# Kernel optimization log

Measured on AMD Instinct MI355X. Metric: run time of the kernel, lower is better.

The kernel has to match this reference:

```python
import jax, jax.numpy as jnp
import numpy as np

B, S, E, NH = 4, 1024, 512, 8
D = E // NH

def layer_norm(x, scale, bias, eps=1e-5):
    mu = jnp.mean(x, -1, keepdims=True)
    var = jnp.mean((x - mu) ** 2, -1, keepdims=True)
    return (x - mu) * jax.lax.rsqrt(var + eps) * scale + bias

def mha(qx, kx, vx, qw, qb, kw, kb, vw, vb, ow, ob, temp):
    b, sq, e = qx.shape
    sk = kx.shape[1]
    q = (qx @ qw + qb).reshape(b, sq, NH, D)
    k = (kx @ kw + kb).reshape(b, sk, NH, D)
    v = (vx @ vw + vb).reshape(b, sk, NH, D)
    scores = jnp.einsum('bqhd,bkhd->bhqk', q, k) * (D ** -0.5) / temp
    w = jax.nn.softmax(scores, axis=-1)  # dropout is identity in eval mode
    o = jnp.einsum('bhqk,bkhd->bqhd', w, v).reshape(b, sq, e)
    return o @ ow + ob

def setup_inputs():
    key = jax.random.key(0)
    ks = jax.random.split(key, 10)
    sc = 0.02  # init scale for weights
    return {
        'body_feats': jax.random.normal(ks[0], (B, S, E), jnp.float32),
        'limb_feats': jax.random.normal(ks[1], (B, S, E), jnp.float32),
        'attn_qw': jax.random.normal(ks[2], (4, E, E), jnp.float32) * sc,
        'attn_qb': jnp.zeros((4, E), jnp.float32),
        'attn_kw': jax.random.normal(ks[3], (4, E, E), jnp.float32) * sc,
        'attn_kb': jnp.zeros((4, E), jnp.float32),
        'attn_vw': jax.random.normal(ks[4], (4, E, E), jnp.float32) * sc,
        'attn_vb': jnp.zeros((4, E), jnp.float32),
        'attn_ow': jax.random.normal(ks[5], (4, E, E), jnp.float32) * sc,
        'attn_ob': jnp.zeros((4, E), jnp.float32),
        'ffn_w1': jax.random.normal(ks[6], (2, E, 4 * E), jnp.float32) * sc,
        'ffn_b1': jnp.zeros((2, 4 * E), jnp.float32),
        'ffn_w2': jax.random.normal(ks[7], (2, 4 * E, E), jnp.float32) * sc,
        'ffn_b2': jnp.zeros((2, E), jnp.float32),
        'norm_scale': jnp.ones((6, E), jnp.float32),
        'norm_bias': jnp.zeros((6, E), jnp.float32),
        'gate_w': jax.random.normal(ks[8], (2 * E, 2), jnp.float32) * sc,
        'gate_b': jnp.zeros((2,), jnp.float32),
        'temperature': 1,
    }

def reference(body_feats, limb_feats, attn_qw, attn_qb, attn_kw, attn_kb, attn_vw, attn_vb, attn_ow, attn_ob, ffn_w1, ffn_b1, ffn_w2, ffn_b2, norm_scale, norm_bias, gate_w, gate_b, temperature):
    temp = jnp.float32(temperature)
    # attn index: 0=self_body 1=self_limb 2=body2limb 3=limb2body
    # norm index: 0=norm1_body 1=norm2_body 2=norm3_body 3=norm1_limb 4=norm2_limb 5=norm3_limb
    def attn(i, qx, kx, vx):
        return mha(qx, kx, vx, attn_qw[i], attn_qb[i], attn_kw[i], attn_kb[i], attn_vw[i], attn_vb[i], attn_ow[i], attn_ob[i], temp)
    def ffn(i, x):
        return jax.nn.gelu(x @ ffn_w1[i] + ffn_b1[i], approximate=False) @ ffn_w2[i] + ffn_b2[i]
    def ln(i, x):
        return layer_norm(x, norm_scale[i], norm_bias[i])
    body = ln(0, body_feats + attn(0, body_feats, body_feats, body_feats))
    limb = ln(3, limb_feats + attn(1, limb_feats, limb_feats, limb_feats))
    body_cross = attn(2, body, limb, limb)
    limb_cross = attn(3, limb, body, body)
    body_gate = jax.nn.softmax(jnp.concatenate([body, body_cross], -1) @ gate_w + gate_b, axis=-1)
    limb_gate = jax.nn.softmax(jnp.concatenate([limb, limb_cross], -1) @ gate_w + gate_b, axis=-1)
    # NOTE: original torch code applies norm2_body to BOTH streams (preserved faithfully)
    body = ln(1, body * body_gate[..., 0:1] + body_cross * body_gate[..., 1:2])
    limb = ln(1, limb * limb_gate[..., 0:1] + limb_cross * limb_gate[..., 1:2])
    body = ln(2, body + ffn(0, body))
    limb = ln(5, limb + ffn(1, limb))
    return body, limb
```

## Files before the change

kernel.cpp:

```cpp
#include <hip/hip_runtime.h>

#define AS1 __attribute__((address_space(1)))
#define AS3 __attribute__((address_space(3)))

typedef __attribute__((ext_vector_type(4))) float f32x4;
typedef __attribute__((ext_vector_type(8))) short s16x8;

static __device__ __forceinline__ ushort f2bf(float f) {
  union { float f; unsigned u; } x; x.f = f;
  unsigned r = x.u + 0x7FFFu + ((x.u >> 16) & 1u);
  return (ushort)(r >> 16);
}
static __device__ __forceinline__ float bf2f(ushort u) {
  union { unsigned u; float f; } x; x.u = ((unsigned)u) << 16; return x.f;
}
static __device__ __forceinline__ float ex2(float x) {
  return __builtin_amdgcn_exp2f(x);
}
static __device__ __forceinline__ unsigned cvt_pk_bf16(float a, float b) {
  unsigned r;
  asm("v_cvt_pk_bf16_f32 %0, %1, %2" : "=v"(r) : "v"(a), "v"(b));
  return r;
}
static __device__ __forceinline__ float gelu_fast(float v) {
  float u = 0.7978845608028654f * (v + 0.044715f * v * v * v);
  float e = ex2(u * 2.885390081777927f);
  float r = __builtin_amdgcn_rcpf(e + 1.0f);
  return v - v * r;
}
static __device__ __forceinline__ float parse_scalar(const void* p) {
  int i = *(const int*)p;
  if (i > 0 && i < 1000000) return (float)i;
  union { int i; float f; } u; u.i = i; return u.f;
}

__global__ __launch_bounds__(256)
void transpose_all(const float* __restrict__ qw, const float* __restrict__ kw,
                   const float* __restrict__ vw, const float* __restrict__ ow,
                   const float* __restrict__ w1, const float* __restrict__ w2,
                   const float* __restrict__ body, const float* __restrict__ limb,
                   ushort* __restrict__ FW, ushort* __restrict__ WOT,
                   ushort* __restrict__ W1T, ushort* __restrict__ W2T,
                   ushort* __restrict__ XB, ushort* __restrict__ XL)
{
  __shared__ float tile[32][33];
  int id = blockIdx.x;
  if (id >= 8192) {
    int id2 = id - 8192;
    const float* in = (id2 >= 2048) ? limb : body;
    ushort* out = (id2 >= 2048) ? XL : XB;
    int j = id2 & 2047;
    int t = threadIdx.y * 32 + threadIdx.x;
    int i = (j * 256 + t) * 4;
    float4 v = *(const float4*)(in + i);
    ushort4 o;
    o.x = f2bf(v.x); o.y = f2bf(v.y); o.z = f2bf(v.z); o.w = f2bf(v.w);
    *(ushort4*)(out + i) = o;
    return;
  }
  const float* in; ushort* out; int K, N, tx, ty;
  if (id < 3072) {
    int trip = id / 768, r = id - trip * 768, which = r >> 8, t2 = r & 255;
    int widx = (which == 0) ? trip : (trip ^ (trip >> 1));
    in = ((which == 0) ? qw : (which == 1) ? kw : vw) + (size_t)widx * 512 * 512;
    out = FW + (size_t)trip * 1536 * 512 + (size_t)which * 512 * 512;
    K = 512; N = 512; tx = t2 & 15; ty = t2 >> 4;
  } else if (id < 4096) {
    int r = id - 3072, wi = r >> 8, t2 = r & 255;
    in = ow + (size_t)wi * 512 * 512; out = WOT + (size_t)wi * 512 * 512;
    K = 512; N = 512; tx = t2 & 15; ty = t2 >> 4;
  } else if (id < 6144) {
    int r = id - 4096, s = r >> 10, t2 = r & 1023;
    in = w1 + (size_t)s * 512 * 2048; out = W1T + (size_t)s * 2048 * 512;
    K = 512; N = 2048; tx = t2 & 63; ty = t2 >> 6;
  } else {
    int r = id - 6144, s = r >> 10, t2 = r & 1023;
    in = w2 + (size_t)s * 2048 * 512; out = W2T + (size_t)s * 512 * 2048;
    K = 2048; N = 512; tx = t2 & 15; ty = t2 >> 4;
  }
  int nb = tx * 32, kb = ty * 32;
  int x = threadIdx.x, y = threadIdx.y;
  #pragma unroll
  for (int i = 0; i < 4; ++i)
    tile[y + i * 8][x] = in[(size_t)(kb + y + i * 8) * N + nb + x];
  __syncthreads();
  #pragma unroll
  for (int i = 0; i < 4; ++i)
    out[(size_t)(nb + y + i * 8) * K + kb + x] = f2bf(tile[x][y + i * 8]);
}

struct GemmArgs {
  const ushort* A; const ushort* Bt;
  const float *b0, *b1, *b2;
  float* outf; ushort* outb;
  ushort *qo, *ko, *vto;
  const void* sp;
  int M, N, K, kind;
};

template<int FM, int FN>
__global__ __launch_bounds__(256)
void gemm_k(GemmArgs g0, GemmArgs g1)
{
  constexpr int BM = FM * 32, BN = FN * 32;
  __shared__ ushort As[2][BM * 64];
  __shared__ ushort Bs[2][BN * 64];
  GemmArgs g = blockIdx.z ? g1 : g0;
  const int t = threadIdx.x, lane = t & 63, w = t >> 6;
  const int lr = lane & 15, gq = lane >> 4;
  const int wr = w >> 1, wc = w & 1;
  const int m0 = blockIdx.y * BM, n0 = blockIdx.x * BN;
  const int K = g.K;
  const int nk = K >> 6;

  auto stage = [&](int kt, int buf) {
    #pragma unroll
    for (int p = 0; p < FM; ++p) {
      int c = p * 256 + t, row = c >> 3, sl = c & 7;
      const ushort* src = g.A + (size_t)(m0 + row) * K + kt * 64 + ((sl ^ (row & 7)) << 3);
      __builtin_amdgcn_global_load_lds((const AS1 void*)src,
          (AS3 void*)(As[buf] + (size_t)(p * 256 + (t & ~63)) * 8), 16, 0, 0);
    }
    #pragma unroll
    for (int p = 0; p < FN; ++p) {
      int c = p * 256 + t, row = c >> 3, sl = c & 7;
      const ushort* src = g.Bt + (size_t)(n0 + row) * K + kt * 64 + ((sl ^ (row & 7)) << 3);
      __builtin_amdgcn_global_load_lds((const AS1 void*)src,
          (AS3 void*)(Bs[buf] + (size_t)(p * 256 + (t & ~63)) * 8), 16, 0, 0);
    }
  };

  f32x4 acc[FM][FN];
  f32x4 zero = {0.f, 0.f, 0.f, 0.f};
  #pragma unroll
  for (int m = 0; m < FM; ++m)
    #pragma unroll
    for (int n = 0; n < FN; ++n) acc[m][n] = zero;

  stage(0, 0);
  __syncthreads();
  for (int kt = 0; kt < nk; ++kt) {
    int cur = kt & 1;
    const ushort* Ab = As[cur];
    const ushort* Bb = Bs[cur];
    if (kt + 1 < nk) stage(kt + 1, cur ^ 1);
    #pragma unroll
    for (int ks = 0; ks < 2; ++ks) {
      s16x8 af[FM], bfv[FN];
      #pragma unroll
      for (int m = 0; m < FM; ++m) {
        int row = wr * (FM * 16) + m * 16 + lr;
        af[m] = *(const s16x8*)(Ab + row * 64 + (((ks * 4 + gq) ^ (row & 7)) << 3));
      }
      #pragma unroll
      for (int n = 0; n < FN; ++n) {
        int row = wc * (FN * 16) + n * 16 + lr;
        bfv[n] = *(const s16x8*)(Bb + row * 64 + (((ks * 4 + gq) ^ (row & 7)) << 3));
      }
      __builtin_amdgcn_s_setprio(1);
      #pragma unroll
      for (int m = 0; m < FM; ++m)
        #pragma unroll
        for (int n = 0; n < FN; ++n)
          acc[m][n] = __builtin_amdgcn_mfma_f32_16x16x32_bf16(af[m], bfv[n], acc[m][n], 0, 0, 0);
      __builtin_amdgcn_s_setprio(0);
    }
    __syncthreads();
  }

  float qs = 1.0f;
  if (g.kind == 3 && g.sp) qs = 0.125f / parse_scalar(g.sp) * 1.4426950408889634f;
  #pragma unroll
  for (int n = 0; n < FN; ++n) {
    int col = n0 + wc * (FN * 16) + n * 16 + lr;
    int seg = col >> 9, cm = col & 511;
    float bv;
    if (g.kind == 3) bv = (seg == 0) ? g.b0[cm] : (seg == 1) ? g.b1[cm] : g.b2[cm];
    else bv = g.b0 ? g.b0[col] : 0.f;
    #pragma unroll
    for (int m = 0; m < FM; ++m) {
      int rowb = m0 + wr * (FM * 16) + m * 16 + 4 * gq;
      if (g.kind == 3) {
        if (seg == 2) {
          int d = cm & 63, hh = cm >> 6, bb = rowb >> 10, s = rowb & 1023;
          ushort4 pk;
          pk.x = f2bf(acc[m][n][0] + bv); pk.y = f2bf(acc[m][n][1] + bv);
          pk.z = f2bf(acc[m][n][2] + bv); pk.w = f2bf(acc[m][n][3] + bv);
          *(ushort4*)(g.vto + (((size_t)(bb * 8 + hh) * 64 + d) << 10) + s) = pk;
        } else if (seg == 1) {
          #pragma unroll
          for (int r = 0; r < 4; ++r)
            g.ko[(size_t)(rowb + r) * 512 + cm] = f2bf(acc[m][n][r] + bv);
        } else {
          #pragma unroll
          for (int r = 0; r < 4; ++r)
            g.qo[(size_t)(rowb + r) * 512 + cm] = f2bf((acc[m][n][r] + bv) * qs);
        }
      } else {
        #pragma unroll
        for (int r = 0; r < 4; ++r) {
          float v = acc[m][n][r] + bv;
          if (g.kind == 2) v = gelu_fast(v);
          if (g.kind == 0) g.outf[(size_t)(rowb + r) * g.N + col] = v;
          else g.outb[(size_t)(rowb + r) * g.N + col] = f2bf(v);
        }
      }
    }
  }
}

__global__ __launch_bounds__(256)
void attn_core(const ushort* __restrict__ Q0, const ushort* __restrict__ K0,
               const ushort* __restrict__ V0, ushort* __restrict__ O0,
               const ushort* __restrict__ Q1, const ushort* __restrict__ K1,
               const ushort* __restrict__ V1, ushort* __restrict__ O1)
{
  __shared__ ushort Ks[2][64 * 64];
  __shared__ ushort Vs[2][64 * 64];
  __shared__ ushort Ps[4][1024];
  const int str = blockIdx.y;
  const ushort* Q = str ? Q1 : Q0;
  const ushort* Kx = str ? K1 : K0;
  const ushort* VT = str ? V1 : V0;
  ushort* O = str ? O1 : O0;

  const int t = threadIdx.x, lane = t & 63, w = t >> 6;
  const int lr = lane & 15, g = lane >> 4;
  int bid = blockIdx.x;
  int L = (bid & 7) * 64 + (bid >> 3);
  int bh = L >> 4, qt = L & 15;
  size_t tbase = ((size_t)(bh >> 3) << 19) + ((size_t)(bh & 7) << 6);
  const ushort* Kbase = Kx + tbase;
  const ushort* Vbase = VT + ((size_t)bh << 16);
  int q0 = qt * 64 + w * 16;
  char* myPs = (char*)Ps[w];
  const int psw = (lr & 7) << 4;

  auto stage = [&](int kt, int buf) {
    #pragma unroll
    for (int p = 0; p < 2; ++p) {
      int c = p * 256 + t, row = c >> 3, sl = c & 7;
      const ushort* src = Kbase + (size_t)(kt * 64 + row) * 512 + ((sl ^ (row & 7)) << 3);
      __builtin_amdgcn_global_load_lds((const AS1 void*)src,
          (AS3 void*)(Ks[buf] + (size_t)(p * 256 + (t & ~63)) * 8), 16, 0, 0);
    }
    #pragma unroll
    for (int p = 0; p < 2; ++p) {
      int c = p * 256 + t, row = c >> 3, sl = c & 7;
      const ushort* src = Vbase + (size_t)row * 1024 + kt * 64 + ((sl ^ (row & 7)) << 3);
      __builtin_amdgcn_global_load_lds((const AS1 void*)src,
          (AS3 void*)(Vs[buf] + (size_t)(p * 256 + (t & ~63)) * 8), 16, 0, 0);
    }
  };

  s16x8 qf[2];
  #pragma unroll
  for (int ks = 0; ks < 2; ++ks)
    qf[ks] = *(const s16x8*)(Q + tbase + (size_t)(q0 + lr) * 512 + ks * 32 + g * 8);

  f32x4 po[4];
  f32x4 zero = {0.f, 0.f, 0.f, 0.f};
  #pragma unroll
  for (int dt = 0; dt < 4; ++dt) po[dt] = zero;
  float mrow = -1e30f, lsum = 0.f;

  stage(0, 0);
  __syncthreads();
  #pragma unroll 2
  for (int kt = 0; kt < 16; ++kt) {
    int cur = kt & 1;
    const ushort* Kb = Ks[cur];
    const ushort* Vb = Vs[cur];
    if (kt < 15) stage(kt + 1, cur ^ 1);

    f32x4 sc[4];
    #pragma unroll
    for (int c = 0; c < 4; ++c) {
      sc[c] = zero;
      #pragma unroll
      for (int ks = 0; ks < 2; ++ks) {
        int row = c * 16 + lr;
        s16x8 kf = *(const s16x8*)(Kb + row * 64 + (((ks * 4 + g) ^ (row & 7)) << 3));
        sc[c] = __builtin_amdgcn_mfma_f32_16x16x32_bf16(kf, qf[ks], sc[c], 0, 0, 0);
      }
    }

    float tm = sc[0][0];
    #pragma unroll
    for (int c = 0; c < 4; ++c)
      #pragma unroll
      for (int r = 0; r < 4; ++r) tm = fmaxf(tm, sc[c][r]);
    tm = fmaxf(tm, __shfl_xor(tm, 16));
    tm = fmaxf(tm, __shfl_xor(tm, 32));
    float nm = fmaxf(mrow, tm);
    float fr = ex2(mrow - nm);
    float ts = 0.f;
    #pragma unroll
    for (int c = 0; c < 4; ++c)
      #pragma unroll
      for (int r = 0; r < 4; ++r) {
        float pv = ex2(sc[c][r] - nm);
        sc[c][r] = pv;
        ts += pv;
      }
    ts += __shfl_xor(ts, 16);
    ts += __shfl_xor(ts, 32);
    lsum = lsum * fr + ts;
    mrow = nm;
    #pragma unroll
    for (int dt = 0; dt < 4; ++dt) po[dt] *= fr;

    #pragma unroll
    for (int c = 0; c < 4; ++c) {
      uint2 d;
      d.x = cvt_pk_bf16(sc[c][0], sc[c][1]);
      d.y = cvt_pk_bf16(sc[c][2], sc[c][3]);
      *(uint2*)(myPs + lr * 128 + ((c * 32 + g * 8) ^ psw)) = d;
    }
    s16x8 paf[2];
    #pragma unroll
    for (int ks = 0; ks < 2; ++ks)
      paf[ks] = *(const s16x8*)(myPs + lr * 128 + ((ks * 64 + g * 16) ^ psw));

    __builtin_amdgcn_s_setprio(1);
    #pragma unroll
    for (int dt = 0; dt < 4; ++dt) {
      int vrow = dt * 16 + lr;
      #pragma unroll
      for (int ks = 0; ks < 2; ++ks) {
        s16x8 vf = *(const s16x8*)(Vb + vrow * 64 + (((ks * 4 + g) ^ (vrow & 7)) << 3));
        po[dt] = __builtin_amdgcn_mfma_f32_16x16x32_bf16(vf, paf[ks], po[dt], 0, 0, 0);
      }
    }
    __builtin_amdgcn_s_setprio(0);
    __syncthreads();
  }

  float inv = 1.0f / lsum;
  #pragma unroll
  for (int dt = 0; dt < 4; ++dt) {
    ushort4 pk;
    pk.x = f2bf(po[dt][0] * inv);
    pk.y = f2bf(po[dt][1] * inv);
    pk.z = f2bf(po[dt][2] * inv);
    pk.w = f2bf(po[dt][3] * inv);
    *(ushort4*)(O + tbase + (size_t)(q0 + lr) * 512 + dt * 16 + 4 * g) = pk;
  }
}

__global__ __launch_bounds__(256)
void add_ln_fb2(const float* __restrict__ a0, const ushort* __restrict__ b0,
                ushort* __restrict__ o0, const float* __restrict__ a1,
                const ushort* __restrict__ b1, ushort* __restrict__ o1,
                const float* __restrict__ nsc, const float* __restrict__ nbi,
                int i0, int i1)
{
  const float* a = blockIdx.y ? a1 : a0;
  const ushort* b = blockIdx.y ? b1 : b0;
  ushort* outb = blockIdx.y ? o1 : o0;
  const float* scale = nsc + (blockIdx.y ? i1 : i0) * 512;
  const float* bias = nbi + (blockIdx.y ? i1 : i0) * 512;
  const int lane = threadIdx.x & 63, w = threadIdx.x >> 6;
  const size_t row = blockIdx.x * 4 + w;
  s16x8 bv8 = *(const s16x8*)(b + row * 512 + lane * 8);
  float x[8];
  #pragma unroll
  for (int j = 0; j < 8; j += 4) {
    float4 av = *(const float4*)(a + row * 512 + lane * 8 + j);
    x[j] = av.x + bf2f((ushort)bv8[j]);
    x[j + 1] = av.y + bf2f((ushort)bv8[j + 1]);
    x[j + 2] = av.z + bf2f((ushort)bv8[j + 2]);
    x[j + 3] = av.w + bf2f((ushort)bv8[j + 3]);
  }
  float s = 0.f, ss = 0.f;
  #pragma unroll
  for (int j = 0; j < 8; ++j) { s += x[j]; ss += x[j] * x[j]; }
  #pragma unroll
  for (int m = 1; m < 64; m <<= 1) { s += __shfl_xor(s, m); ss += __shfl_xor(ss, m); }
  float mu = s * (1.f / 512.f);
  float rstd = rsqrtf(ss * (1.f / 512.f) - mu * mu + 1e-5f);
  ushort o[8];
  #pragma unroll
  for (int j = 0; j < 8; ++j) {
    int e = lane * 8 + j;
    o[j] = f2bf((x[j] - mu) * rstd * scale[e] + bias[e]);
  }
  *(s16x8*)(outb + row * 512 + lane * 8) = *(s16x8*)o;
}

__global__ __launch_bounds__(256)
void add_ln_bb2(const ushort* __restrict__ a0, const ushort* __restrict__ b0,
                float* __restrict__ o0, const ushort* __restrict__ a1,
                const ushort* __restrict__ b1, float* __restrict__ o1,
                const float* __restrict__ nsc, const float* __restrict__ nbi,
                int i0, int i1)
{
  const ushort* a = blockIdx.y ? a1 : a0;
  const ushort* b = blockIdx.y ? b1 : b0;
  float* outf = blockIdx.y ? o1 : o0;
  const float* scale = nsc + (blockIdx.y ? i1 : i0) * 512;
  const float* bias = nbi + (blockIdx.y ? i1 : i0) * 512;
  const int lane = threadIdx.x & 63, w = threadIdx.x >> 6;
  const size_t row = blockIdx.x * 4 + w;
  s16x8 av = *(const s16x8*)(a + row * 512 + lane * 8);
  s16x8 bv = *(const s16x8*)(b + row * 512 + lane * 8);
  float x[8];
  #pragma unroll
  for (int j = 0; j < 8; ++j)
    x[j] = bf2f((ushort)av[j]) + bf2f((ushort)bv[j]);
  float s = 0.f, ss = 0.f;
  #pragma unroll
  for (int j = 0; j < 8; ++j) { s += x[j]; ss += x[j] * x[j]; }
  #pragma unroll
  for (int m = 1; m < 64; m <<= 1) { s += __shfl_xor(s, m); ss += __shfl_xor(ss, m); }
  float mu = s * (1.f / 512.f);
  float rstd = rsqrtf(ss * (1.f / 512.f) - mu * mu + 1e-5f);
  float o[8];
  #pragma unroll
  for (int j = 0; j < 8; ++j) {
    int e = lane * 8 + j;
    o[j] = (x[j] - mu) * rstd * scale[e] + bias[e];
  }
  *(float4*)(outf + row * 512 + lane * 8) = *(float4*)o;
  *(float4*)(outf + row * 512 + lane * 8 + 4) = *(float4*)(o + 4);
}

__global__ __launch_bounds__(256)
void gate_ln2(const ushort* __restrict__ x0, const ushort* __restrict__ c0,
              ushort* __restrict__ o0, const ushort* __restrict__ x1,
              const ushort* __restrict__ c1, ushort* __restrict__ o1,
              const float* __restrict__ gw, const float* __restrict__ gb,
              const float* __restrict__ scale, const float* __restrict__ bias)
{
  const ushort* x = blockIdx.y ? x1 : x0;
  const ushort* cr = blockIdx.y ? c1 : c0;
  ushort* outb = blockIdx.y ? o1 : o0;
  const int lane = threadIdx.x & 63, w = threadIdx.x >> 6;
  const size_t row = blockIdx.x * 4 + w;
  s16x8 xv8 = *(const s16x8*)(x + row * 512 + lane * 8);
  s16x8 cv8 = *(const s16x8*)(cr + row * 512 + lane * 8);
  float xv[8], cv[8];
  #pragma unroll
  for (int j = 0; j < 8; ++j) { xv[j] = bf2f((ushort)xv8[j]); cv[j] = bf2f((ushort)cv8[j]); }
  float d0 = 0.f, d1 = 0.f;
  #pragma unroll
  for (int j = 0; j < 8; ++j) {
    int e = lane * 8 + j;
    float2 g0 = *(const float2*)(gw + 2 * e);
    float2 g1 = *(const float2*)(gw + 2 * (512 + e));
    d0 += xv[j] * g0.x + cv[j] * g1.x;
    d1 += xv[j] * g0.y + cv[j] * g1.y;
  }
  #pragma unroll
  for (int m = 1; m < 64; m <<= 1) { d0 += __shfl_xor(d0, m); d1 += __shfl_xor(d1, m); }
  d0 += gb[0]; d1 += gb[1];
  float mx = fmaxf(d0, d1);
  float e0 = __expf(d0 - mx), e1 = __expf(d1 - mx);
  float inv = 1.0f / (e0 + e1);
  float g0w = e0 * inv, g1w = e1 * inv;
  float xc[8];
  float s = 0.f, ss = 0.f;
  #pragma unroll
  for (int j = 0; j < 8; ++j) {
    xc[j] = xv[j] * g0w + cv[j] * g1w;
    s += xc[j]; ss += xc[j] * xc[j];
  }
  #pragma unroll
  for (int m = 1; m < 64; m <<= 1) { s += __shfl_xor(s, m); ss += __shfl_xor(ss, m); }
  float mu = s * (1.f / 512.f);
  float rstd = rsqrtf(ss * (1.f / 512.f) - mu * mu + 1e-5f);
  ushort o[8];
  #pragma unroll
  for (int j = 0; j < 8; ++j) {
    int e = lane * 8 + j;
    o[j] = f2bf((xc[j] - mu) * rstd * scale[e] + bias[e]);
  }
  *(s16x8*)(outb + row * 512 + lane * 8) = *(s16x8*)o;
}

extern "C" void kernel_launch(void* const* d_in, const int* in_sizes, int n_in,
                              void* d_out, int out_size, void* d_ws, size_t ws_size,
                              hipStream_t stream)
{
  (void)in_sizes; (void)n_in; (void)out_size; (void)ws_size;
  const int T = 4096, E = 512, HD = 2048;
  const float* body = (const float*)d_in[0];
  const float* limb = (const float*)d_in[1];
  const float* qw = (const float*)d_in[2];  const float* qb = (const float*)d_in[3];
  const float* kw = (const float*)d_in[4];  const float* kb = (const float*)d_in[5];
  const float* vw = (const float*)d_in[6];  const float* vb = (const float*)d_in[7];
  const float* ow = (const float*)d_in[8];  const float* ob = (const float*)d_in[9];
  const float* w1 = (const float*)d_in[10]; const float* fb1 = (const float*)d_in[11];
  const float* w2 = (const float*)d_in[12]; const float* fb2 = (const float*)d_in[13];
  const float* nsc = (const float*)d_in[14]; const float* nbi = (const float*)d_in[15];
  const float* gw = (const float*)d_in[16];  const float* gb = (const float*)d_in[17];
  const void* temp = d_in[18];

  char* ws = (char*)d_ws;
  size_t off = 0;
  auto alloc = [&](size_t b) { char* p = ws + off; off += (b + 255) & ~(size_t)255; return p; };
  ushort* FW    = (ushort*)alloc((size_t)4 * 1536 * 512 * 2);
  ushort* WOT   = (ushort*)alloc((size_t)4 * E * E * 2);
  ushort* W1T   = (ushort*)alloc((size_t)2 * E * HD * 2);
  ushort* W2T   = (ushort*)alloc((size_t)2 * HD * E * 2);
  ushort* XB    = (ushort*)alloc((size_t)T * E * 2);
  ushort* XL    = (ushort*)alloc((size_t)T * E * 2);
  ushort* PROJA = (ushort*)alloc((size_t)T * E * 2);
  ushort* PROJB = (ushort*)alloc((size_t)T * E * 2);
  ushort* BODYb = (ushort*)alloc((size_t)T * E * 2);
  ushort* LIMBb = (ushort*)alloc((size_t)T * E * 2);
  ushort* BCRb  = (ushort*)alloc((size_t)T * E * 2);
  ushort* LCRb  = (ushort*)alloc((size_t)T * E * 2);
  ushort* GBb   = (ushort*)alloc((size_t)T * E * 2);
  ushort* GLb   = (ushort*)alloc((size_t)T * E * 2);
  ushort* QA    = (ushort*)alloc((size_t)T * E * 2);
  ushort* KA    = (ushort*)alloc((size_t)T * E * 2);
  ushort* VTA   = (ushort*)alloc((size_t)T * E * 2);
  ushort* QB    = (ushort*)alloc((size_t)T * E * 2);
  ushort* KB    = (ushort*)alloc((size_t)T * E * 2);
  ushort* VTB   = (ushort*)alloc((size_t)T * E * 2);
  ushort* AOA   = (ushort*)alloc((size_t)T * E * 2);
  ushort* AOB   = (ushort*)alloc((size_t)T * E * 2);
  ushort* H1A   = QA;
  ushort* H1B   = KB;
  ushort* F2A   = PROJA;
  ushort* F2B   = PROJB;

  transpose_all<<<12288, dim3(32, 8), 0, stream>>>(qw, kw, vw, ow, w1, w2, body, limb,
                                                   FW, WOT, W1T, W2T, XB, XL);

  auto qkv_pair = [&](const ushort* A0, int t0, ushort* q0, ushort* k0, ushort* v0,
                      const ushort* A1, int t1, ushort* q1, ushort* k1, ushort* v1) {
    GemmArgs a{}, b{};
    int kv0 = t0 ^ (t0 >> 1), kv1 = t1 ^ (t1 >> 1);
    a.A = A0; a.Bt = FW + (size_t)t0 * 1536 * 512;
    a.b0 = qb + t0 * E; a.b1 = kb + kv0 * E; a.b2 = vb + kv0 * E;
    a.qo = q0; a.ko = k0; a.vto = v0; a.sp = temp; a.M = T; a.N = 1536; a.K = E; a.kind = 3;
    b = a;
    b.A = A1; b.Bt = FW + (size_t)t1 * 1536 * 512;
    b.b0 = qb + t1 * E; b.b1 = kb + kv1 * E; b.b2 = vb + kv1 * E;
    b.qo = q1; b.ko = k1; b.vto = v1;
    gemm_k<4, 4><<<dim3(12, 32, 2), 256, 0, stream>>>(a, b);
  };
  auto oproj_pair = [&](const ushort* A0, int i0, ushort* ob0,
                        const ushort* A1, int i1, ushort* ob1) {
    GemmArgs a{}, b{};
    a.A = A0; a.Bt = WOT + (size_t)i0 * E * E; a.b0 = ob + i0 * E;
    a.outb = ob0; a.M = T; a.N = E; a.K = E; a.kind = 1;
    b = a;
    b.A = A1; b.Bt = WOT + (size_t)i1 * E * E; b.b0 = ob + i1 * E;
    b.outb = ob1;
    gemm_k<2, 2><<<dim3(8, 64, 2), 256, 0, stream>>>(a, b);
  };

  qkv_pair(XB, 0, QA, KA, VTA, XL, 1, QB, KB, VTB);
  attn_core<<<dim3(512, 2), 256, 0, stream>>>(QA, KA, VTA, AOA, QB, KB, VTB, AOB);
  oproj_pair(AOA, 0, PROJA, AOB, 1, PROJB);
  add_ln_fb2<<<dim3(T / 4, 2), 256, 0, stream>>>(body, PROJA, BODYb, limb, PROJB, LIMBb,
                                                 nsc, nbi, 0, 3);
  qkv_pair(BODYb, 2, QA, KA, VTA, LIMBb, 3, QB, KB, VTB);
  attn_core<<<dim3(512, 2), 256, 0, stream>>>(QA, KB, VTB, AOA, QB, KA, VTA, AOB);
  oproj_pair(AOA, 2, BCRb, AOB, 3, LCRb);

  gate_ln2<<<dim3(T / 4, 2), 256, 0, stream>>>(BODYb, BCRb, GBb, LIMBb, LCRb, GLb,
                                               gw, gb, nsc + E, nbi + E);

  {
    GemmArgs a{}, b{};
    a.A = GBb; a.Bt = W1T; a.b0 = fb1; a.outb = H1A;
    a.M = T; a.N = HD; a.K = E; a.kind = 2;
    b = a; b.A = GLb; b.Bt = W1T + (size_t)HD * E; b.b0 = fb1 + HD; b.outb = H1B;
    gemm_k<4, 4><<<dim3(16, 32, 2), 256, 0, stream>>>(a, b);
  }
  {
    GemmArgs a{}, b{};
    a.A = H1A; a.Bt = W2T; a.b0 = fb2; a.outb = F2A;
    a.M = T; a.N = E; a.K = HD; a.kind = 1;
    b = a; b.A = H1B; b.Bt = W2T + (size_t)HD * E; b.b0 = fb2 + E; b.outb = F2B;
    gemm_k<2, 2><<<dim3(8, 64, 2), 256, 0, stream>>>(a, b);
  }
  add_ln_bb2<<<dim3(T / 4, 2), 256, 0, stream>>>(GBb, F2A, (float*)d_out,
                                                 GLb, F2B, (float*)d_out + (size_t)T * E,
                                                 nsc, nbi, 2, 5);
}
```

Measured before the change: 377.4 us.

## Single-buffer GEMM LDS, add XCD block swizzle, widen N tiles for E-output GEMMs

The bf16 GEMM kernel drops its double-buffered LDS staging for a single buffer: each k-step now loads its tile, synchronises, then computes. This halves shared memory per block, which may allow more resident blocks, but removes the overlap of the next tile's loads with the current MFMAs. Block indices are remapped with a stride-8 swizzle so neighbouring tiles are spread across the MI355X's XCDs, aiming for better L2 reuse. The output-projection and second FFN GEMMs switch from 2x2 to 2x4 fragment tiles, giving fewer, wider blocks.

```diff
diff --git a/kernel.cpp b/kernel.cpp
--- a/kernel.cpp
+++ b/kernel.cpp
@@ -103,30 +103,37 @@
 void gemm_k(GemmArgs g0, GemmArgs g1)
 {
   constexpr int BM = FM * 32, BN = FN * 32;
-  __shared__ ushort As[2][BM * 64];
-  __shared__ ushort Bs[2][BN * 64];
-  GemmArgs g = blockIdx.z ? g1 : g0;
+  __shared__ ushort As[BM * 64];
+  __shared__ ushort Bs[BN * 64];
+  const int nx = gridDim.x, nxy = nx * gridDim.y;
+  const int nwg = nxy * gridDim.z;
+  int bid = blockIdx.x + nx * blockIdx.y + nxy * blockIdx.z;
+  int sw = (nwg & 7) ? bid : ((bid & 7) * (nwg >> 3) + (bid >> 3));
+  const int bz = sw / nxy;
+  int r2 = sw - bz * nxy;
+  const int by = r2 / nx, bx = r2 - by * nx;
+  GemmArgs g = bz ? g1 : g0;
   const int t = threadIdx.x, lane = t & 63, w = t >> 6;
   const int lr = lane & 15, gq = lane >> 4;
   const int wr = w >> 1, wc = w & 1;
-  const int m0 = blockIdx.y * BM, n0 = blockIdx.x * BN;
+  const int m0 = by * BM, n0 = bx * BN;
   const int K = g.K;
   const int nk = K >> 6;
 
-  auto stage = [&](int kt, int buf) {
+  auto stage = [&](int kt) {
     #pragma unroll
     for (int p = 0; p < FM; ++p) {
       int c = p * 256 + t, row = c >> 3, sl = c & 7;
       const ushort* src = g.A + (size_t)(m0 + row) * K + kt * 64 + ((sl ^ (row & 7)) << 3);
       __builtin_amdgcn_global_load_lds((const AS1 void*)src,
-          (AS3 void*)(As[buf] + (size_t)(p * 256 + (t & ~63)) * 8), 16, 0, 0);
+          (AS3 void*)(As + (size_t)(p * 256 + (t & ~63)) * 8), 16, 0, 0);
     }
     #pragma unroll
     for (int p = 0; p < FN; ++p) {
       int c = p * 256 + t, row = c >> 3, sl = c & 7;
       const ushort* src = g.Bt + (size_t)(n0 + row) * K + kt * 64 + ((sl ^ (row & 7)) << 3);
       __builtin_amdgcn_global_load_lds((const AS1 void*)src,
-          (AS3 void*)(Bs[buf] + (size_t)(p * 256 + (t & ~63)) * 8), 16, 0, 0);
+          (AS3 void*)(Bs + (size_t)(p * 256 + (t & ~63)) * 8), 16, 0, 0);
     }
   };
 
@@ -137,25 +144,21 @@
     #pragma unroll
     for (int n = 0; n < FN; ++n) acc[m][n] = zero;
 
-  stage(0, 0);
-  __syncthreads();
   for (int kt = 0; kt < nk; ++kt) {
-    int cur = kt & 1;
-    const ushort* Ab = As[cur];
-    const ushort* Bb = Bs[cur];
-    if (kt + 1 < nk) stage(kt + 1, cur ^ 1);
+    stage(kt);
+    __syncthreads();
     #pragma unroll
     for (int ks = 0; ks < 2; ++ks) {
       s16x8 af[FM], bfv[FN];
       #pragma unroll
       for (int m = 0; m < FM; ++m) {
         int row = wr * (FM * 16) + m * 16 + lr;
-        af[m] = *(const s16x8*)(Ab + row * 64 + (((ks * 4 + gq) ^ (row & 7)) << 3));
+        af[m] = *(const s16x8*)(As + row * 64 + (((ks * 4 + gq) ^ (row & 7)) << 3));
       }
       #pragma unroll
       for (int n = 0; n < FN; ++n) {
         int row = wc * (FN * 16) + n * 16 + lr;
-        bfv[n] = *(const s16x8*)(Bb + row * 64 + (((ks * 4 + gq) ^ (row & 7)) << 3));
+        bfv[n] = *(const s16x8*)(Bs + row * 64 + (((ks * 4 + gq) ^ (row & 7)) << 3));
       }
       __builtin_amdgcn_s_setprio(1);
       #pragma unroll
@@ -550,7 +553,7 @@
     b = a;
     b.A = A1; b.Bt = WOT + (size_t)i1 * E * E; b.b0 = ob + i1 * E;
     b.outb = ob1;
-    gemm_k<2, 2><<<dim3(8, 64, 2), 256, 0, stream>>>(a, b);
+    gemm_k<2, 4><<<dim3(4, 64, 2), 256, 0, stream>>>(a, b);
   };
 
   qkv_pair(XB, 0, QA, KA, VTA, XL, 1, QB, KB, VTB);
@@ -577,7 +580,7 @@
     a.A = H1A; a.Bt = W2T; a.b0 = fb2; a.outb = F2A;
     a.M = T; a.N = E; a.K = HD; a.kind = 1;
     b = a; b.A = H1B; b.Bt = W2T + (size_t)HD * E; b.b0 = fb2 + E; b.outb = F2B;
-    gemm_k<2, 2><<<dim3(8, 64, 2), 256, 0, stream>>>(a, b);
+    gemm_k<2, 4><<<dim3(4, 64, 2), 256, 0, stream>>>(a, b);
   }
   add_ln_bb2<<<dim3(T / 4, 2), 256, 0, stream>>>(GBb, F2A, (float*)d_out,
                                                  GLb, F2B, (float*)d_out + (size_t)T * E,
```

Measured after the change: 369.3 us. -2.2%, faster.
